# Kernel optimization log

Hardware: AMD Instinct MI355X
Metric: run time of the kernel (lower is better)

Reference implementation:

```python
import jax, jax.numpy as jnp
import numpy as np

BETA = 1.0  # inverse temperature (default of retrieve())
EPS = 1e-12  # matches torch F.normalize eps


def _l2_normalize(x):
    # torch.nn.functional.normalize(p=2, dim=-1): x / max(||x||, eps)
    n = jnp.sqrt(jnp.sum(x * x, axis=-1, keepdims=True))
    return x / jnp.maximum(n, EPS)


def setup_inputs() -> dict:
    key = jax.random.key(0)
    kq, kk = jax.random.split(key)
    N, K, D = 65536, 4096, 128
    queries = jax.random.normal(kq, (N, D), dtype=jnp.float32)
    # learnable memory keys, init_std = 0.02
    keys = jax.random.normal(kk, (K, D), dtype=jnp.float32) * 0.02
    return {"queries": queries, "keys": keys}


def reference(queries, keys):
    # normalize_keys=True, normalize_queries=True
    k_n = _l2_normalize(keys)
    q_n = _l2_normalize(queries)
    # values are TIED to the raw keys parameter (get_values returns self.keys,
    # un-normalized) — only the score-side keys are normalized.
    values = keys
    scores = BETA * jnp.einsum('nd,kd->nk', q_n, k_n)  # [N, K]
    attention = jax.nn.softmax(scores, axis=-1)
    retrieved = jnp.einsum('nk,kd->nd', attention, values)  # [N, D]
    return retrieved
```

## Files before the change

### kernel.cpp

```cpp
#include <hip/hip_runtime.h>
#include <hip/hip_bf16.h>
#include <stdint.h>


typedef __attribute__((ext_vector_type(8))) short bf16x8;
typedef __attribute__((ext_vector_type(16))) float f32x16;

#define MFMA32(a, b, c) __builtin_amdgcn_mfma_f32_32x32x16_bf16(a, b, c, 0, 0, 0)
#define ASYNC_CP16(gsrc, ldst)                                                  \
  __builtin_amdgcn_global_load_lds(                                             \
      (const __attribute__((address_space(1))) void*)(gsrc),                    \
      (__attribute__((address_space(3))) void*)(ldst), 16, 0, 0)

__device__ __forceinline__ unsigned pkbf(float lo, float hi) {
  union { __hip_bfloat162 h2; unsigned u; } v;
  v.h2 = __float22bfloat162_rn(float2{lo, hi});
  return v.u;
}

__global__ __launch_bounds__(256) void prep_k(const float* __restrict__ k,
                                              char* __restrict__ knf,
                                              char* __restrict__ vtf, int K) {
  __shared__ float sRaw[64 * 132];
  __shared__ float sScale[64];
  const int tid = threadIdx.x;
  const int kbase = blockIdx.x * 64;
  {
    const int key_loc = tid >> 2, dq = tid & 3;
    const float4* src = (const float4*)(k + (size_t)(kbase + key_loc) * 128 + dq * 32);
    float4 f[8];
    float ss = 0.f;
#pragma unroll
    for (int i = 0; i < 8; ++i) {
      f[i] = src[i];
      ss += f[i].x * f[i].x + f[i].y * f[i].y + f[i].z * f[i].z + f[i].w * f[i].w;
    }
    ss += __shfl_xor(ss, 1);
    ss += __shfl_xor(ss, 2);
    float4* dst = (float4*)(sRaw + key_loc * 132 + dq * 32);
#pragma unroll
    for (int i = 0; i < 8; ++i) dst[i] = f[i];
    if (dq == 0) sScale[key_loc] = ss > 0.f ? rsqrtf(ss) : 0.f;
  }
  __syncthreads();

#pragma unroll
  for (int r = 0; r < 4; ++r) {
    const int c = r * 256 + tid;
    const int t_loc = c >> 9, ds = (c >> 6) & 7, l = c & 63;
    const int h5 = l >> 5, c32 = l & 31;
    const int key_loc = t_loc * 32 + c32;
    const float sc = sScale[key_loc];
    const float* p = sRaw + key_loc * 132 + ds * 16 + h5 * 8;
    uint4 w;
    w.x = pkbf(p[0] * sc, p[1] * sc);
    w.y = pkbf(p[2] * sc, p[3] * sc);
    w.z = pkbf(p[4] * sc, p[5] * sc);
    w.w = pkbf(p[6] * sc, p[7] * sc);
    *(uint4*)(knf + ((size_t)blockIdx.x * 1024 + c) * 16) = w;
  }
#pragma unroll
  for (int r = 0; r < 4; ++r) {
    const int c = r * 256 + tid;
    const int s = c >> 8, db2 = (c >> 6) & 3, l = c & 63;
    const int h5 = l >> 5, c32 = l & 31;
    const int d = db2 * 32 + c32;
    const int kb = (s >> 1) * 32 + (s & 1) * 8 + h5 * 4;
    float f[8];
#pragma unroll
    for (int j = 0; j < 8; ++j)
      f[j] = sRaw[(kb + (j & 3) + (j >> 2) * 16) * 132 + d];
    uint4 w;
    w.x = pkbf(f[0], f[1]);
    w.y = pkbf(f[2], f[3]);
    w.z = pkbf(f[4], f[5]);
    w.w = pkbf(f[6], f[7]);
    *(uint4*)(vtf + ((size_t)blockIdx.x * 1024 + c) * 16) = w;
  }
}

__global__ __launch_bounds__(256, 2) void attn_main(
    const float* __restrict__ q, const char* __restrict__ knf,
    const char* __restrict__ vtf, float* __restrict__ out, int K) {
  __shared__ __align__(16) char sK[2][16384];
  const int tid = threadIdx.x;
  const int wave = tid >> 6, lane = tid & 63;
  const int h5 = lane >> 5, c32 = lane & 31;
  const int qrow0 = blockIdx.x * 128 + wave * 32;

  bf16x8 qf[8];
  {
    const float* qr = q + (size_t)(qrow0 + c32) * 128;
    float f[64];
    float ss = 0.f;
#pragma unroll
    for (int ds = 0; ds < 8; ++ds) {
      const float4 a = *(const float4*)(qr + ds * 16 + h5 * 8);
      const float4 b = *(const float4*)(qr + ds * 16 + h5 * 8 + 4);
      f[ds * 8 + 0] = a.x; f[ds * 8 + 1] = a.y; f[ds * 8 + 2] = a.z; f[ds * 8 + 3] = a.w;
      f[ds * 8 + 4] = b.x; f[ds * 8 + 5] = b.y; f[ds * 8 + 6] = b.z; f[ds * 8 + 7] = b.w;
    }
#pragma unroll
    for (int i = 0; i < 64; ++i) ss += f[i] * f[i];
    ss += __shfl_xor(ss, 32);
    const float sc = (ss > 0.f ? rsqrtf(ss) : 0.f) * 1.44269504f;
#pragma unroll
    for (int ds = 0; ds < 8; ++ds) {
      union { unsigned u[4]; bf16x8 v; } t;
#pragma unroll
      for (int p = 0; p < 4; ++p)
        t.u[p] = pkbf(f[ds * 8 + 2 * p] * sc, f[ds * 8 + 2 * p + 1] * sc);
      qf[ds] = t.v;
    }
  }

  f32x16 acc[4];
#pragma unroll
  for (int db2 = 0; db2 < 4; ++db2)
#pragma unroll
    for (int r = 0; r < 16; ++r) acc[db2][r] = 0.f;
  float den = 0.f;

  const int nIter = K >> 6;
  auto stage = [&](int it, int buf) {
#pragma unroll
    for (int i = 0; i < 4; ++i)
      ASYNC_CP16(knf + (size_t)it * 16384 + (wave * 4 + i) * 1024 + lane * 16,
                 sK[buf] + (wave * 4 + i) * 1024);
  };

  stage(0, 0);
  for (int it = 0; it < nIter; ++it) {
    const int buf = it & 1;
    __syncthreads();
    if (it + 1 < nIter) stage(it + 1, buf ^ 1);

    f32x16 S[2];
#pragma unroll
    for (int t = 0; t < 2; ++t) {
      f32x16 s;
#pragma unroll
      for (int r = 0; r < 16; ++r) s[r] = 0.f;
#pragma unroll
      for (int ds = 0; ds < 8; ++ds) {
        const bf16x8 kf = *(const bf16x8*)(sK[buf] + (t * 8 + ds) * 1024 + lane * 16);
        s = MFMA32(kf, qf[ds], s);
      }
      S[t] = s;
    }

    const char* vbase = vtf + (size_t)it * 16384;
    bf16x8 vcur[4], vnxt[4];
#pragma unroll
    for (int db2 = 0; db2 < 4; ++db2)
      vcur[db2] = *(const bf16x8*)(vbase + db2 * 1024 + lane * 16);
#pragma unroll
    for (int s = 0; s < 4; ++s) {
      if (s < 3)
#pragma unroll
        for (int db2 = 0; db2 < 4; ++db2)
          vnxt[db2] = *(const bf16x8*)(vbase + ((s + 1) * 4 + db2) * 1024 + lane * 16);
      const int t = s >> 1, w = s & 1;
      float e[8];
#pragma unroll
      for (int j = 0; j < 8; ++j) {
        const int rr = w * 4 + (j & 3) + (j >> 2) * 8;
        e[j] = __builtin_amdgcn_exp2f(S[t][rr]);
      }
      den += ((e[0] + e[1]) + (e[2] + e[3])) + ((e[4] + e[5]) + (e[6] + e[7]));
      union { unsigned u[4]; bf16x8 v; } pf;
#pragma unroll
      for (int j2 = 0; j2 < 4; ++j2) pf.u[j2] = pkbf(e[2 * j2], e[2 * j2 + 1]);
#pragma unroll
      for (int db2 = 0; db2 < 4; ++db2)
        acc[db2] = MFMA32(vcur[db2], pf.v, acc[db2]);
      if (s < 3)
#pragma unroll
        for (int db2 = 0; db2 < 4; ++db2) vcur[db2] = vnxt[db2];
    }
  }

  den += __shfl_xor(den, 32);
  const float rd = 1.0f / den;

  __syncthreads();
  float* wls = (float*)(&sK[0][0] + wave * 4096);
#pragma unroll
  for (int db2 = 0; db2 < 4; ++db2) {
#pragma unroll
    for (int qd = 0; qd < 4; ++qd) {
      float4 v;
      v.x = acc[db2][qd * 4 + 0] * rd;
      v.y = acc[db2][qd * 4 + 1] * rd;
      v.z = acc[db2][qd * 4 + 2] * rd;
      v.w = acc[db2][qd * 4 + 3] * rd;
      *(float4*)(wls + c32 * 32 + (((h5 + 2 * qd) ^ (c32 & 7)) << 2)) = v;
    }
#pragma unroll
    for (int p = 0; p < 4; ++p) {
      const int ql = p * 8 + (lane >> 3);
      const int x = lane & 7;
      const float4 v = *(const float4*)(wls + ql * 32 + ((x ^ (ql & 7)) << 2));
      *(float4*)(out + (size_t)(qrow0 + ql) * 128 + db2 * 32 + x * 4) = v;
    }
  }
}

extern "C" void kernel_launch(void* const* d_in, const int* in_sizes, int n_in,
                              void* d_out, int out_size, void* d_ws, size_t ws_size,
                              hipStream_t stream) {
  const float* q = (const float*)d_in[0];
  const float* k = (const float*)d_in[1];
  const int N = in_sizes[0] / 128;
  const int K = in_sizes[1] / 128;
  char* ws = (char*)d_ws;
  char* knf = ws;
  char* vtf = ws + (size_t)K * 256;
  float* out = (float*)d_out;

  prep_k<<<dim3(K / 64), dim3(256), 0, stream>>>(k, knf, vtf, K);
  attn_main<<<dim3(N / 128), dim3(256), 0, stream>>>(q, knf, vtf, out, K);
}
```

Before: 222.2 us.

## Split output head dimension across two blocks and raise occupancy

Adds a second grid dimension that splits the 128-wide value/output dimension into two halves. Each block now recomputes the full QK scores and softmax exponentials but keeps only half the PV accumulators. The freed registers allow launch bounds of 4 blocks per CU instead of 2. In exchange, the QK MFMA work, the exp work and the K tile streaming are all duplicated across the two splits.

New measurement: 335.2 us. +50.8%, slower.

```diff
diff --git a/kernel.cpp b/kernel.cpp
--- a/kernel.cpp
+++ b/kernel.cpp
@@ -79,13 +79,14 @@
   }
 }
 
-__global__ __launch_bounds__(256, 2) void attn_main(
+__global__ __launch_bounds__(256, 4) void attn_main(
     const float* __restrict__ q, const char* __restrict__ knf,
     const char* __restrict__ vtf, float* __restrict__ out, int K) {
   __shared__ __align__(16) char sK[2][16384];
   const int tid = threadIdx.x;
   const int wave = tid >> 6, lane = tid & 63;
   const int h5 = lane >> 5, c32 = lane & 31;
+  const int split = blockIdx.y;
   const int qrow0 = blockIdx.x * 128 + wave * 32;
 
   bf16x8 qf[8];
@@ -114,11 +115,11 @@
     }
   }
 
-  f32x16 acc[4];
-#pragma unroll
-  for (int db2 = 0; db2 < 4; ++db2)
-#pragma unroll
-    for (int r = 0; r < 16; ++r) acc[db2][r] = 0.f;
+  f32x16 acc[2];
+#pragma unroll
+  for (int dt = 0; dt < 2; ++dt)
+#pragma unroll
+    for (int r = 0; r < 16; ++r) acc[dt][r] = 0.f;
   float den = 0.f;
 
   const int nIter = K >> 6;
@@ -128,55 +129,46 @@
       ASYNC_CP16(knf + (size_t)it * 16384 + (wave * 4 + i) * 1024 + lane * 16,
                  sK[buf] + (wave * 4 + i) * 1024);
   };
+  const char* vsp = vtf + split * 2048;
 
   stage(0, 0);
   for (int it = 0; it < nIter; ++it) {
     const int buf = it & 1;
     __syncthreads();
     if (it + 1 < nIter) stage(it + 1, buf ^ 1);
-
-    f32x16 S[2];
+    const size_t vit = (size_t)it * 16384;
+
 #pragma unroll
     for (int t = 0; t < 2; ++t) {
-      f32x16 s;
-#pragma unroll
-      for (int r = 0; r < 16; ++r) s[r] = 0.f;
+      bf16x8 vf[4];
+#pragma unroll
+      for (int w = 0; w < 2; ++w)
+#pragma unroll
+        for (int dt = 0; dt < 2; ++dt)
+          vf[w * 2 + dt] = *(const bf16x8*)(vsp + vit + (t * 2 + w) * 4096 +
+                                            dt * 1024 + lane * 16);
+      f32x16 S = {};
 #pragma unroll
       for (int ds = 0; ds < 8; ++ds) {
         const bf16x8 kf = *(const bf16x8*)(sK[buf] + (t * 8 + ds) * 1024 + lane * 16);
-        s = MFMA32(kf, qf[ds], s);
+        S = MFMA32(kf, qf[ds], S);
       }
-      S[t] = s;
-    }
-
-    const char* vbase = vtf + (size_t)it * 16384;
-    bf16x8 vcur[4], vnxt[4];
-#pragma unroll
-    for (int db2 = 0; db2 < 4; ++db2)
-      vcur[db2] = *(const bf16x8*)(vbase + db2 * 1024 + lane * 16);
-#pragma unroll
-    for (int s = 0; s < 4; ++s) {
-      if (s < 3)
-#pragma unroll
-        for (int db2 = 0; db2 < 4; ++db2)
-          vnxt[db2] = *(const bf16x8*)(vbase + ((s + 1) * 4 + db2) * 1024 + lane * 16);
-      const int t = s >> 1, w = s & 1;
-      float e[8];
-#pragma unroll
-      for (int j = 0; j < 8; ++j) {
-        const int rr = w * 4 + (j & 3) + (j >> 2) * 8;
-        e[j] = __builtin_amdgcn_exp2f(S[t][rr]);
+#pragma unroll
+      for (int w = 0; w < 2; ++w) {
+        float e[8];
+#pragma unroll
+        for (int j = 0; j < 8; ++j) {
+          const int rr = w * 4 + (j & 3) + (j >> 2) * 8;
+          e[j] = __builtin_amdgcn_exp2f(S[rr]);
+        }
+        den += ((e[0] + e[1]) + (e[2] + e[3])) + ((e[4] + e[5]) + (e[6] + e[7]));
+        union { unsigned u[4]; bf16x8 v; } pf;
+#pragma unroll
+        for (int j2 = 0; j2 < 4; ++j2) pf.u[j2] = pkbf(e[2 * j2], e[2 * j2 + 1]);
+#pragma unroll
+        for (int dt = 0; dt < 2; ++dt)
+          acc[dt] = MFMA32(vf[w * 2 + dt], pf.v, acc[dt]);
       }
-      den += ((e[0] + e[1]) + (e[2] + e[3])) + ((e[4] + e[5]) + (e[6] + e[7]));
-      union { unsigned u[4]; bf16x8 v; } pf;
-#pragma unroll
-      for (int j2 = 0; j2 < 4; ++j2) pf.u[j2] = pkbf(e[2 * j2], e[2 * j2 + 1]);
-#pragma unroll
-      for (int db2 = 0; db2 < 4; ++db2)
-        acc[db2] = MFMA32(vcur[db2], pf.v, acc[db2]);
-      if (s < 3)
-#pragma unroll
-        for (int db2 = 0; db2 < 4; ++db2) vcur[db2] = vnxt[db2];
     }
   }
 
@@ -186,14 +178,14 @@
   __syncthreads();
   float* wls = (float*)(&sK[0][0] + wave * 4096);
 #pragma unroll
-  for (int db2 = 0; db2 < 4; ++db2) {
+  for (int dt = 0; dt < 2; ++dt) {
 #pragma unroll
     for (int qd = 0; qd < 4; ++qd) {
       float4 v;
-      v.x = acc[db2][qd * 4 + 0] * rd;
-      v.y = acc[db2][qd * 4 + 1] * rd;
-      v.z = acc[db2][qd * 4 + 2] * rd;
-      v.w = acc[db2][qd * 4 + 3] * rd;
+      v.x = acc[dt][qd * 4 + 0] * rd;
+      v.y = acc[dt][qd * 4 + 1] * rd;
+      v.z = acc[dt][qd * 4 + 2] * rd;
+      v.w = acc[dt][qd * 4 + 3] * rd;
       *(float4*)(wls + c32 * 32 + (((h5 + 2 * qd) ^ (c32 & 7)) << 2)) = v;
     }
 #pragma unroll
@@ -201,7 +193,7 @@
       const int ql = p * 8 + (lane >> 3);
       const int x = lane & 7;
       const float4 v = *(const float4*)(wls + ql * 32 + ((x ^ (ql & 7)) << 2));
-      *(float4*)(out + (size_t)(qrow0 + ql) * 128 + db2 * 32 + x * 4) = v;
+      *(float4*)(out + (size_t)(qrow0 + ql) * 128 + split * 64 + dt * 32 + x * 4) = v;
     }
   }
 }
@@ -219,5 +211,5 @@
   float* out = (float*)d_out;
 
   prep_k<<<dim3(K / 64), dim3(256), 0, stream>>>(k, knf, vtf, K);
-  attn_main<<<dim3(N / 128), dim3(256), 0, stream>>>(q, knf, vtf, out, K);
-}
+  attn_main<<<dim3(N / 128, 2), dim3(256), 0, stream>>>(q, knf, vtf, out, K);
+}
```
